# Kernel tuning notes

Measured on AMD Instinct MI355X. Metric: run time of the kernel, lower is better.

The kernel has to match this reference:

```python
import math
import jax, jax.numpy as jnp
import numpy as np

Q_MAX = 127.0  # 2**(8-1) - 1 for n_bits=8
SCALE_EPS = 1e-5


def _hadamard_matrix(n):
    H = np.array([[1.0]], dtype=np.float32)
    while H.shape[0] < n:
        H = np.block([[H, H], [H, -H]])
    return jnp.asarray(H)


def quantize_per_channel_absmax(w):
    # per output-channel absmax quantize-dequantize (torch weight per_channel)
    scales = jnp.clip(jnp.max(jnp.abs(w), axis=-1, keepdims=True) / Q_MAX, SCALE_EPS, None)
    return jnp.round(w / scales) * scales


def quantize_per_token_absmax(x):
    # per-token (last-dim) absmax quantize-dequantize
    scales = jnp.clip(jnp.max(jnp.abs(x), axis=-1, keepdims=True) / Q_MAX, SCALE_EPS, None)
    return jnp.round(x / scales) * scales


def setup_inputs() -> dict:
    key = jax.random.key(0)
    k1, k2, k3 = jax.random.split(key, 3)
    B, S, D_IN, D_OUT = 2, 2048, 4096, 4096
    x = jax.random.normal(k1, (B, S, D_IN), dtype=jnp.float32)
    # weight quantized at __init__ time (per_channel, 8-bit), as in the wrapper
    weight = quantize_per_channel_absmax(
        jax.random.normal(k2, (D_OUT, D_IN), dtype=jnp.float32) * (1.0 / math.sqrt(D_IN)))
    bias = jax.random.normal(k3, (D_OUT,), dtype=jnp.float32)
    return {"x": x, "weight": weight, "bias": bias, "had_dim": 64}


def reference(x, weight, bias, had_dim):
    # --- online_partial_had, K == 1 path ---
    B, S, D = x.shape
    n_groups = D // had_dim
    H = _hadamard_matrix(n_groups).astype(x.dtype)
    xr = x.reshape(-1, n_groups, had_dim)  # (B*S, G, had_dim)
    # hadamard_transform along the group axis, scale = 1/sqrt(G)
    xr = jnp.einsum('hg,bgd->bhd', H, xr) * (1.0 / math.sqrt(n_groups))
    x = xr.reshape(B, S, D)
    # --- per-token absmax activation quant ---
    x = quantize_per_token_absmax(x)
    # --- linear with (already quantized) weight ---
    return jnp.einsum('bsd,od->bso', x, weight) + bias
```

## Files before the change

kernel.cpp:

```cpp
#include <hip/hip_runtime.h>
#include <hip/hip_bf16.h>

#define M_DIM 4096
#define N_DIM 4096
#define K_DIM 4096

typedef __attribute__((ext_vector_type(4))) int i32x4;
typedef __attribute__((ext_vector_type(16))) int i32x16;

typedef __attribute__((address_space(1))) const void GV;
typedef __attribute__((address_space(3))) void LV;

__global__ __launch_bounds__(256) void prequant_kernel(const float* __restrict__ x,
                                                       const float* __restrict__ w,
                                                       char* __restrict__ xq,
                                                       char* __restrict__ wq,
                                                       float* __restrict__ sx,
                                                       float* __restrict__ sw) {
  const int wave = threadIdx.x >> 6;
  const int lane = threadIdx.x & 63;

  if (blockIdx.x >= 1024) {
    const int row = (blockIdx.x - 1024) * 4 + wave;
    const float* wp = w + (size_t)row * 4096;
    float4 v[16];
#pragma unroll
    for (int c = 0; c < 16; ++c) v[c] = *(const float4*)(wp + c * 256 + lane * 4);
    float amax = 0.f;
#pragma unroll
    for (int c = 0; c < 16; ++c)
      amax = fmaxf(amax, fmaxf(fmaxf(fabsf(v[c].x), fabsf(v[c].y)),
                               fmaxf(fabsf(v[c].z), fabsf(v[c].w))));
#pragma unroll
    for (int off = 32; off >= 1; off >>= 1) amax = fmaxf(amax, __shfl_xor(amax, off, 64));
    amax = fmaxf(amax, 1e-30f);
    const float inv = 127.0f / amax;
    char* op = wq + (size_t)row * 4096;
#pragma unroll
    for (int c = 0; c < 16; ++c) {
      char4 o;
      o.x = (char)rintf(v[c].x * inv);
      o.y = (char)rintf(v[c].y * inv);
      o.z = (char)rintf(v[c].z * inv);
      o.w = (char)rintf(v[c].w * inv);
      *(char4*)(op + c * 256 + lane * 4) = o;
    }
    if (lane == 0) sw[row] = amax * (1.0f / 127.0f);
    return;
  }

  const int tok = blockIdx.x * 4 + wave;
  const int gs = lane >> 4;
  const int q = lane & 15;
  const float* xp = x + (size_t)tok * 4096;

  float4 v[16];
#pragma unroll
  for (int gl = 0; gl < 16; ++gl)
    v[gl] = *(const float4*)(xp + (gl * 4 + gs) * 64 + q * 4);

#pragma unroll
  for (int s = 1; s < 16; s <<= 1) {
#pragma unroll
    for (int i = 0; i < 16; ++i) {
      if ((i & s) == 0) {
        float4 a = v[i], b = v[i | s];
        v[i].x = a.x + b.x; v[i].y = a.y + b.y; v[i].z = a.z + b.z; v[i].w = a.w + b.w;
        v[i | s].x = a.x - b.x; v[i | s].y = a.y - b.y;
        v[i | s].z = a.z - b.z; v[i | s].w = a.w - b.w;
      }
    }
  }
#pragma unroll
  for (int st = 0; st < 2; ++st) {
    const int L = 16 << st;
    const bool hi = (lane & L) != 0;
#pragma unroll
    for (int i = 0; i < 16; ++i) {
      float4 t;
      t.x = __shfl_xor(v[i].x, L, 64);
      t.y = __shfl_xor(v[i].y, L, 64);
      t.z = __shfl_xor(v[i].z, L, 64);
      t.w = __shfl_xor(v[i].w, L, 64);
      if (hi) {
        v[i].x = t.x - v[i].x; v[i].y = t.y - v[i].y;
        v[i].z = t.z - v[i].z; v[i].w = t.w - v[i].w;
      } else {
        v[i].x += t.x; v[i].y += t.y; v[i].z += t.z; v[i].w += t.w;
      }
    }
  }

  float amax = 0.f;
#pragma unroll
  for (int i = 0; i < 16; ++i) {
    v[i].x *= 0.125f; v[i].y *= 0.125f; v[i].z *= 0.125f; v[i].w *= 0.125f;
    amax = fmaxf(amax, fmaxf(fmaxf(fabsf(v[i].x), fabsf(v[i].y)),
                             fmaxf(fabsf(v[i].z), fabsf(v[i].w))));
  }
#pragma unroll
  for (int off = 32; off >= 1; off >>= 1) amax = fmaxf(amax, __shfl_xor(amax, off, 64));

  const float s = fmaxf(amax * (1.0f / 127.0f), 1e-5f);
  const float inv = 1.0f / s;

  char* op = xq + (size_t)tok * 4096;
#pragma unroll
  for (int gl = 0; gl < 16; ++gl) {
    char4 o;
    o.x = (char)rintf(v[gl].x * inv);
    o.y = (char)rintf(v[gl].y * inv);
    o.z = (char)rintf(v[gl].z * inv);
    o.w = (char)rintf(v[gl].w * inv);
    *(char4*)(op + (gl * 4 + gs) * 64 + q * 4) = o;
  }
  if (lane == 0) sx[tok] = s;
}

__global__ __launch_bounds__(256, 3) void gemm_i8(const char* __restrict__ A,
                                                  const char* __restrict__ B,
                                                  const float* __restrict__ sx,
                                                  const float* __restrict__ sw,
                                                  const float* __restrict__ bias,
                                                  float* __restrict__ C) {
  __shared__ char As[128 * 128];
  __shared__ char Bs[128 * 128];

  const int tid = threadIdx.x;
  const int lane = tid & 63;
  const int wave = tid >> 6;
  const int bm = blockIdx.y, bn = blockIdx.x;
  const int wm = wave >> 1, wn = wave & 1;

  const int trow = tid >> 3;
  const int tseg = (tid & 7) ^ (trow & 7);
  const char* gA = A + (size_t)(bm * 128 + trow) * K_DIM + tseg * 16;
  const char* gB = B + (size_t)(bn * 128 + trow) * K_DIM + tseg * 16;
  char* lA = &As[tid * 16];
  char* lB = &Bs[tid * 16];

  const int m32 = lane & 31;
  const int half = lane >> 5;
  const int aBase = (wm * 64 + m32) * 128;
  const int bBase = (wn * 64 + m32) * 128;
  int sl[4];
#pragma unroll
  for (int kc = 0; kc < 4; ++kc) sl[kc] = ((kc * 2 + half) ^ (m32 & 7)) * 16;

  i32x16 acc[2][2];
#pragma unroll
  for (int i = 0; i < 2; ++i)
#pragma unroll
    for (int j = 0; j < 2; ++j)
#pragma unroll
      for (int r = 0; r < 16; ++r) acc[i][j][r] = 0;

  for (int kt = 0; kt < K_DIM / 128; ++kt) {
    __syncthreads();
    const size_t ke = (size_t)kt * 128;
#pragma unroll
    for (int c = 0; c < 4; ++c) {
      __builtin_amdgcn_global_load_lds((GV*)(gA + ke + (size_t)c * 32 * K_DIM),
                                       (LV*)(lA + c * 4096), 16, 0, 0);
      __builtin_amdgcn_global_load_lds((GV*)(gB + ke + (size_t)c * 32 * K_DIM),
                                       (LV*)(lB + c * 4096), 16, 0, 0);
    }
    __syncthreads();

#pragma unroll
    for (int kc = 0; kc < 4; ++kc) {
      i32x4 a0 = *(const i32x4*)&As[aBase + sl[kc]];
      i32x4 a1 = *(const i32x4*)&As[aBase + 4096 + sl[kc]];
      i32x4 b0 = *(const i32x4*)&Bs[bBase + sl[kc]];
      i32x4 b1 = *(const i32x4*)&Bs[bBase + 4096 + sl[kc]];
      acc[0][0] = __builtin_amdgcn_mfma_i32_32x32x32_i8(a0, b0, acc[0][0], 0, 0, 0);
      acc[0][1] = __builtin_amdgcn_mfma_i32_32x32x32_i8(a0, b1, acc[0][1], 0, 0, 0);
      acc[1][0] = __builtin_amdgcn_mfma_i32_32x32x32_i8(a1, b0, acc[1][0], 0, 0, 0);
      acc[1][1] = __builtin_amdgcn_mfma_i32_32x32x32_i8(a1, b1, acc[1][1], 0, 0, 0);
    }
  }

  float swv[2], bv[2];
#pragma unroll
  for (int j = 0; j < 2; ++j) {
    const int colg = bn * 128 + wn * 64 + j * 32 + m32;
    swv[j] = sw[colg];
    bv[j] = bias[colg];
  }

#pragma unroll
  for (int i = 0; i < 2; ++i) {
    const int rbase = bm * 128 + wm * 64 + i * 32 + 4 * half;
    float sxv[16];
#pragma unroll
    for (int r = 0; r < 16; ++r) sxv[r] = sx[rbase + (r & 3) + 8 * (r >> 2)];
#pragma unroll
    for (int j = 0; j < 2; ++j) {
      const int colg = bn * 128 + wn * 64 + j * 32 + m32;
#pragma unroll
      for (int r = 0; r < 16; ++r) {
        const int rowg = rbase + (r & 3) + 8 * (r >> 2);
        C[(size_t)rowg * N_DIM + colg] = (float)acc[i][j][r] * (sxv[r] * swv[j]) + bv[j];
      }
    }
  }
}

extern "C" void kernel_launch(void* const* d_in, const int* in_sizes, int n_in,
                              void* d_out, int out_size, void* d_ws, size_t ws_size,
                              hipStream_t stream) {
  const float* x = (const float*)d_in[0];
  const float* w = (const float*)d_in[1];
  const float* bias = (const float*)d_in[2];

  char* xq = (char*)d_ws;
  char* wq = xq + (size_t)M_DIM * K_DIM;
  float* sx = (float*)(wq + (size_t)N_DIM * K_DIM);
  float* sw = sx + M_DIM;
  float* out = (float*)d_out;

  prequant_kernel<<<2048, 256, 0, stream>>>(x, w, xq, wq, sx, sw);

  dim3 grid(N_DIM / 128, M_DIM / 128);
  gemm_i8<<<grid, 256, 0, stream>>>(xq, wq, sx, sw, bias, out);
}
```

Before: 251.0 us.

## Restructure int8 GEMM to 256x256 tiles with 4-stage LDS pipeline

The int8 GEMM moves from 128x128 tiles with 256 threads to 256x256 tiles with 512 threads (8 waves, 128x64 per wave). K is now staged in 32-wide slices through a 4-buffer LDS ring, with the next loads issued ahead and explicit vmcnt waits, barriers and setprio around the MFMA block. Blocks are remapped with a 1D swizzle, presumably to improve L2 locality. The aim is to raise arithmetic intensity and hide global load latency. In exchange there are more barriers per K step, 256 blocks to fill the CUs, and hand-written waitcnt ordering that must be correct.

```diff
diff --git a/kernel.cpp b/kernel.cpp
--- a/kernel.cpp
+++ b/kernel.cpp
@@ -1,5 +1,4 @@
 #include <hip/hip_runtime.h>
-#include <hip/hip_bf16.h>
 
 #define M_DIM 4096
 #define N_DIM 4096
@@ -117,90 +116,120 @@
   if (lane == 0) sx[tok] = s;
 }
 
-__global__ __launch_bounds__(256, 3) void gemm_i8(const char* __restrict__ A,
+__global__ __launch_bounds__(512, 2) void gemm_i8(const char* __restrict__ A,
                                                   const char* __restrict__ B,
                                                   const float* __restrict__ sx,
                                                   const float* __restrict__ sw,
                                                   const float* __restrict__ bias,
                                                   float* __restrict__ C) {
-  __shared__ char As[128 * 128];
-  __shared__ char Bs[128 * 128];
+  __shared__ __align__(16) char sm[65536];
 
   const int tid = threadIdx.x;
   const int lane = tid & 63;
   const int wave = tid >> 6;
-  const int bm = blockIdx.y, bn = blockIdx.x;
-  const int wm = wave >> 1, wn = wave & 1;
-
-  const int trow = tid >> 3;
-  const int tseg = (tid & 7) ^ (trow & 7);
-  const char* gA = A + (size_t)(bm * 128 + trow) * K_DIM + tseg * 16;
-  const char* gB = B + (size_t)(bn * 128 + trow) * K_DIM + tseg * 16;
-  char* lA = &As[tid * 16];
-  char* lB = &Bs[tid * 16];
-
+  const int wm = wave >> 2;
+  const int wn = wave & 3;
   const int m32 = lane & 31;
   const int half = lane >> 5;
-  const int aBase = (wm * 64 + m32) * 128;
-  const int bBase = (wn * 64 + m32) * 128;
-  int sl[4];
-#pragma unroll
-  for (int kc = 0; kc < 4; ++kc) sl[kc] = ((kc * 2 + half) ^ (m32 & 7)) * 16;
-
-  i32x16 acc[2][2];
-#pragma unroll
-  for (int i = 0; i < 2; ++i)
+
+  const int bid = blockIdx.x;
+  const int cx = bid & 7, ii = bid >> 3;
+  const int bm = (cx & 3) * 4 + (ii >> 3);
+  const int bn = (cx >> 2) * 8 + (ii & 7);
+
+  const int strow = tid >> 1;
+  const int stseg = ((tid & 1) ^ ((tid >> 3) & 1)) << 4;
+  const char* gA = A + (size_t)(bm * 256 + strow) * K_DIM + stseg;
+  const char* gB = B + (size_t)(bn * 256 + strow) * K_DIM + stseg;
+
+  auto lof = [&](int row) { return row * 32 + ((half ^ ((row >> 2) & 1)) << 4); };
+  const int aoff0 = lof(wm * 128 + 0 + m32);
+  const int aoff1 = lof(wm * 128 + 32 + m32);
+  const int aoff2 = lof(wm * 128 + 64 + m32);
+  const int aoff3 = lof(wm * 128 + 96 + m32);
+  const int boff0 = 8192 + lof(wn * 64 + 0 + m32);
+  const int boff1 = 8192 + lof(wn * 64 + 32 + m32);
+
+  i32x16 acc[4][2];
+#pragma unroll
+  for (int i = 0; i < 4; ++i)
 #pragma unroll
     for (int j = 0; j < 2; ++j)
 #pragma unroll
       for (int r = 0; r < 16; ++r) acc[i][j][r] = 0;
 
-  for (int kt = 0; kt < K_DIM / 128; ++kt) {
-    __syncthreads();
-    const size_t ke = (size_t)kt * 128;
-#pragma unroll
-    for (int c = 0; c < 4; ++c) {
-      __builtin_amdgcn_global_load_lds((GV*)(gA + ke + (size_t)c * 32 * K_DIM),
-                                       (LV*)(lA + c * 4096), 16, 0, 0);
-      __builtin_amdgcn_global_load_lds((GV*)(gB + ke + (size_t)c * 32 * K_DIM),
-                                       (LV*)(lB + c * 4096), 16, 0, 0);
-    }
-    __syncthreads();
-
-#pragma unroll
-    for (int kc = 0; kc < 4; ++kc) {
-      i32x4 a0 = *(const i32x4*)&As[aBase + sl[kc]];
-      i32x4 a1 = *(const i32x4*)&As[aBase + 4096 + sl[kc]];
-      i32x4 b0 = *(const i32x4*)&Bs[bBase + sl[kc]];
-      i32x4 b1 = *(const i32x4*)&Bs[bBase + 4096 + sl[kc]];
-      acc[0][0] = __builtin_amdgcn_mfma_i32_32x32x32_i8(a0, b0, acc[0][0], 0, 0, 0);
-      acc[0][1] = __builtin_amdgcn_mfma_i32_32x32x32_i8(a0, b1, acc[0][1], 0, 0, 0);
-      acc[1][0] = __builtin_amdgcn_mfma_i32_32x32x32_i8(a1, b0, acc[1][0], 0, 0, 0);
-      acc[1][1] = __builtin_amdgcn_mfma_i32_32x32x32_i8(a1, b1, acc[1][1], 0, 0, 0);
-    }
-  }
-
-  float swv[2], bv[2];
-#pragma unroll
-  for (int j = 0; j < 2; ++j) {
-    const int colg = bn * 128 + wn * 64 + j * 32 + m32;
-    swv[j] = sw[colg];
-    bv[j] = bias[colg];
-  }
-
-#pragma unroll
-  for (int i = 0; i < 2; ++i) {
-    const int rbase = bm * 128 + wm * 64 + i * 32 + 4 * half;
+#pragma unroll
+  for (int s = 0; s < 3; ++s) {
+    char* ld = sm + s * 16384 + (tid << 4);
+    const size_t ko = (size_t)s * 32;
+    __builtin_amdgcn_global_load_lds((GV*)(gA + ko), (LV*)ld, 16, 0, 0);
+    __builtin_amdgcn_global_load_lds((GV*)(gB + ko), (LV*)(ld + 8192), 16, 0, 0);
+  }
+  asm volatile("s_waitcnt vmcnt(4)" ::: "memory");
+  __builtin_amdgcn_s_barrier();
+
+#define KTILE(T, DOSTAGE, TAILWAIT)                                                   \
+  {                                                                                   \
+    const char* bufp = sm + ((T) & 3) * 16384;                                        \
+    if (DOSTAGE) {                                                                    \
+      char* ld = sm + (((T) + 3) & 3) * 16384 + (tid << 4);                           \
+      const size_t ko = (size_t)((T) + 3) * 32;                                       \
+      __builtin_amdgcn_global_load_lds((GV*)(gA + ko), (LV*)ld, 16, 0, 0);            \
+      __builtin_amdgcn_global_load_lds((GV*)(gB + ko), (LV*)(ld + 8192), 16, 0, 0);   \
+    }                                                                                 \
+    const i32x4 a0 = *(const i32x4*)(bufp + aoff0);                                   \
+    const i32x4 a1 = *(const i32x4*)(bufp + aoff1);                                   \
+    const i32x4 a2 = *(const i32x4*)(bufp + aoff2);                                   \
+    const i32x4 a3 = *(const i32x4*)(bufp + aoff3);                                   \
+    const i32x4 b0 = *(const i32x4*)(bufp + boff0);                                   \
+    const i32x4 b1 = *(const i32x4*)(bufp + boff1);                                   \
+    __builtin_amdgcn_s_barrier();                                                     \
+    asm volatile("s_waitcnt lgkmcnt(0)" ::: "memory");                                \
+    __builtin_amdgcn_sched_barrier(0);                                                \
+    __builtin_amdgcn_s_setprio(1);                                                    \
+    acc[0][0] = __builtin_amdgcn_mfma_i32_32x32x32_i8(a0, b0, acc[0][0], 0, 0, 0);    \
+    acc[0][1] = __builtin_amdgcn_mfma_i32_32x32x32_i8(a0, b1, acc[0][1], 0, 0, 0);    \
+    acc[1][0] = __builtin_amdgcn_mfma_i32_32x32x32_i8(a1, b0, acc[1][0], 0, 0, 0);    \
+    acc[1][1] = __builtin_amdgcn_mfma_i32_32x32x32_i8(a1, b1, acc[1][1], 0, 0, 0);    \
+    acc[2][0] = __builtin_amdgcn_mfma_i32_32x32x32_i8(a2, b0, acc[2][0], 0, 0, 0);    \
+    acc[2][1] = __builtin_amdgcn_mfma_i32_32x32x32_i8(a2, b1, acc[2][1], 0, 0, 0);    \
+    acc[3][0] = __builtin_amdgcn_mfma_i32_32x32x32_i8(a3, b0, acc[3][0], 0, 0, 0);    \
+    acc[3][1] = __builtin_amdgcn_mfma_i32_32x32x32_i8(a3, b1, acc[3][1], 0, 0, 0);    \
+    __builtin_amdgcn_s_setprio(0);                                                    \
+    asm volatile("s_waitcnt " TAILWAIT ::: "memory");                                 \
+    __builtin_amdgcn_s_barrier();                                                     \
+  }
+
+#pragma unroll 1
+  for (int t = 0; t < 125; ++t) {
+    KTILE(t, 1, "vmcnt(4)");
+  }
+  KTILE(125, 0, "vmcnt(2)");
+  KTILE(126, 0, "vmcnt(0)");
+  KTILE(127, 0, "vmcnt(0)");
+#undef KTILE
+
+  const int col0 = bn * 256 + wn * 64 + m32;
+  const float swv0 = sw[col0];
+  const float swv1 = sw[col0 + 32];
+  const float bv0 = bias[col0];
+  const float bv1 = bias[col0 + 32];
+
+#pragma unroll
+  for (int fm = 0; fm < 4; ++fm) {
+    const int rbase = bm * 256 + wm * 128 + fm * 32 + 4 * half;
     float sxv[16];
 #pragma unroll
     for (int r = 0; r < 16; ++r) sxv[r] = sx[rbase + (r & 3) + 8 * (r >> 2)];
 #pragma unroll
-    for (int j = 0; j < 2; ++j) {
-      const int colg = bn * 128 + wn * 64 + j * 32 + m32;
+    for (int fn = 0; fn < 2; ++fn) {
+      const int colg = col0 + fn * 32;
+      const float swb = fn ? swv1 : swv0;
+      const float bvb = fn ? bv1 : bv0;
 #pragma unroll
       for (int r = 0; r < 16; ++r) {
         const int rowg = rbase + (r & 3) + 8 * (r >> 2);
-        C[(size_t)rowg * N_DIM + colg] = (float)acc[i][j][r] * (sxv[r] * swv[j]) + bv[j];
+        C[(size_t)rowg * N_DIM + colg] = (float)acc[fm][fn][r] * (sxv[r] * swb) + bvb;
       }
     }
   }
@@ -221,6 +250,5 @@
 
   prequant_kernel<<<2048, 256, 0, stream>>>(x, w, xq, wq, sx, sw);
 
-  dim3 grid(N_DIM / 128, M_DIM / 128);
-  gemm_i8<<<grid, 256, 0, stream>>>(xq, wq, sx, sw, bias, out);
+  gemm_i8<<<dim3(256), dim3(512), 0, stream>>>(xq, wq, sx, sw, bias, out);
 }
```

Result: slower. 258.8 us (+3.1%).
